# Performance work log

Hardware: AMD Instinct MI355X
Metric: run time of the kernel (lower is better)

The kernel has to match this reference:

```python
import jax, jax.numpy as jnp
import numpy as np

N = 100000      # total nodes in batched graph
E = 1600000     # total edges (avg degree 16)
G = 4096        # number of molecule graphs in the batch
D_IN = 55       # atom feature width (in_features)
H = 128         # hidden_dim
L = 3           # number of GINConv layers


def setup_inputs() -> dict:
    key = jax.random.key(0)
    ks = jax.random.split(key, 10)
    x = jax.random.normal(ks[0], (N, D_IN), dtype=jnp.float32)
    src = jax.random.randint(ks[1], (E,), 0, N)
    dst = jax.random.randint(ks[2], (E,), 0, N)
    graph_ids = jnp.sort(jax.random.randint(ks[3], (N,), 0, G))
    s_in = 1.0 / np.sqrt(D_IN)
    s_h = 1.0 / np.sqrt(H)
    W_fc = jax.random.uniform(ks[4], (D_IN, H), jnp.float32, -s_in, s_in)
    b_fc = jax.random.uniform(ks[5], (H,), jnp.float32, -s_in, s_in)
    W1 = jax.random.uniform(ks[6], (L, H, H), jnp.float32, -s_h, s_h)
    b1 = jax.random.uniform(ks[7], (L, H), jnp.float32, -s_h, s_h)
    W2 = jax.random.uniform(ks[8], (L, H, H), jnp.float32, -s_h, s_h)
    b2 = jax.random.uniform(ks[9], (L, H), jnp.float32, -s_h, s_h)
    return {"x": x, "W_fc": W_fc, "b_fc": b_fc, "W1": W1, "b1": b1,
            "W2": W2, "b2": b2, "src": src, "dst": dst,
            "graph_ids": graph_ids, "n_graphs": G}


def reference(x, W_fc, b_fc, W1, b1, W2, b2, src, dst, graph_ids, n_graphs):
    # node projection: [N, D_IN] -> [N, H]
    h = x @ W_fc + b_fc
    n = h.shape[0]
    for i in range(L):
        agg = jax.ops.segment_sum(h[src], dst, num_segments=n)  # [N, H]
        z = h + agg                                              # (1+eps)*h + agg, eps=0
        z = jnp.maximum(z @ W1[i] + b1[i], 0.0)                  # MLP layer 1 + ReLU
        h = z @ W2[i] + b2[i]                                    # MLP layer 2
    # dgl.sum_nodes: per-graph sum pooling -> [G, H]
    return jax.ops.segment_sum(h, graph_ids, num_segments=n_graphs)
```

## Files before the change

### kernel.cpp

```cpp
#include <hip/hip_runtime.h>

#define DIN 55
#define HD 128
#define EB 8192
#define NBKT 512

typedef unsigned short u16;
typedef unsigned int u32;
typedef _Float16 h8 __attribute__((ext_vector_type(8)));
typedef float f32x4 __attribute__((ext_vector_type(4)));

__device__ __forceinline__ u32 pkh(float a, float b) {
    auto r = __builtin_amdgcn_cvt_pkrtz(a, b);
    union { decltype(r) h; u32 u; } c; c.h = r; return c.u;
}
__device__ __forceinline__ u16 f2h(float v) {
    union { _Float16 f; u16 s; } c; c.f = (_Float16)v; return c.s;
}
__device__ __forceinline__ float h2f(u16 s) {
    union { u16 s; _Float16 f; } c; c.s = s; return (float)c.f;
}
__device__ __forceinline__ float2 h2f2(u32 u) {
    union { u32 v; _Float16 f[2]; } c; c.v = u;
    return make_float2((float)c.f[0], (float)c.f[1]);
}
__device__ __forceinline__ u32 pk8(float a, float b, float c, float d) {
    int p = __builtin_amdgcn_cvt_pk_fp8_f32(a, b, 0, false);
    p = __builtin_amdgcn_cvt_pk_fp8_f32(c, d, p, true);
    return (u32)p;
}
#define ACC8FP8(P, A, B) { \
    auto u0 = __builtin_amdgcn_cvt_pk_f32_fp8((int)(P).x, false); \
    auto u1 = __builtin_amdgcn_cvt_pk_f32_fp8((int)(P).x, true);  \
    auto u2 = __builtin_amdgcn_cvt_pk_f32_fp8((int)(P).y, false); \
    auto u3 = __builtin_amdgcn_cvt_pk_f32_fp8((int)(P).y, true);  \
    A[0] += u0[0]; A[1] += u0[1]; A[2] += u1[0]; A[3] += u1[1];   \
    B[0] += u2[0]; B[1] += u2[1]; B[2] += u3[0]; B[3] += u3[1]; }
__device__ __forceinline__ uint4 up8to16(uint2 p) {
    auto u0 = __builtin_amdgcn_cvt_pk_f32_fp8((int)p.x, false);
    auto u1 = __builtin_amdgcn_cvt_pk_f32_fp8((int)p.x, true);
    auto u2 = __builtin_amdgcn_cvt_pk_f32_fp8((int)p.y, false);
    auto u3 = __builtin_amdgcn_cvt_pk_f32_fp8((int)p.y, true);
    return make_uint4(pkh(u0[0], u0[1]), pkh(u1[0], u1[1]),
                      pkh(u2[0], u2[1]), pkh(u3[0], u3[1]));
}

__global__ __launch_bounds__(256) void prep_kernel(const int* __restrict__ dst,
                                                   int* __restrict__ histT, int E, int nB,
                                                   const float* __restrict__ W1,
                                                   const float* __restrict__ W2,
                                                   const float* __restrict__ Wfc,
                                                   u16* __restrict__ wfrag,
                                                   float* __restrict__ outz, int out_n) {
    __shared__ int hh[NBKT];
    int t = threadIdx.x;
    if (blockIdx.x < (unsigned)nB) {
        int b = blockIdx.x;
        for (int i = t; i < NBKT; i += 256) hh[i] = 0;
        __syncthreads();
        int base = b * EB;
        int end = min(base + EB, E);
        for (int i = base + t; i < end; i += 256) atomicAdd(&hh[dst[i] >> 8], 1);
        __syncthreads();
        for (int k = t; k < NBKT; k += 256) histT[k * nB + b] = hh[k];
        return;
    }
    int bid = blockIdx.x - nB;
    int kc = t >> 6, lane = t & 63;
    if (bid < 48) {
        int m = bid >> 3, ft = bid & 7;
        int l = m >> 1, s = m & 1;
        const float* W = (s ? W2 : W1) + (size_t)l * HD * HD;
        int j = ft * 16 + (lane & 15);
        int k0 = kc * 32 + ((lane >> 4) << 3);
        h8 v;
#pragma unroll
        for (int i = 0; i < 8; i++)
            v[i] = (_Float16)W[(size_t)(k0 + i) * HD + j];
        *(h8*)&wfrag[(((size_t)bid * 4 + kc) * 64 + lane) * 8] = v;
    } else if (bid < 56) {
        if (kc < 2) {
            int ft = bid - 48;
            int j = ft * 16 + (lane & 15);
            int k0 = kc * 32 + ((lane >> 4) << 3);
            h8 v;
#pragma unroll
            for (int i = 0; i < 8; i++) {
                int k = k0 + i;
                v[i] = (k < DIN) ? (_Float16)Wfc[(size_t)k * HD + j] : (_Float16)0.f;
            }
            *(h8*)&wfrag[98304 + (((size_t)(ft * 2 + kc)) * 64 + lane) * 8] = v;
        }
    } else {
        int i = ((bid - 56) * 256 + t) * 2;
        if (i + 1 < out_n) *(float2*)&outz[i] = make_float2(0.f, 0.f);
        else if (i < out_n) outz[i] = 0.f;
    }
}

__global__ __launch_bounds__(256) void scan1_kernel(int* data, int* bsums, int n) {
    __shared__ int sT[256];
    int t = threadIdx.x;
    int base = blockIdx.x * 1024 + t * 4;
    int v0 = (base + 0 < n) ? data[base + 0] : 0;
    int v1 = (base + 1 < n) ? data[base + 1] : 0;
    int v2 = (base + 2 < n) ? data[base + 2] : 0;
    int v3 = (base + 3 < n) ? data[base + 3] : 0;
    v1 += v0; v2 += v1; v3 += v2;
    sT[t] = v3;
    __syncthreads();
    for (int off = 1; off < 256; off <<= 1) {
        int x = (t >= off) ? sT[t - off] : 0;
        __syncthreads();
        sT[t] += x;
        __syncthreads();
    }
    int excl = (t == 0) ? 0 : sT[t - 1];
    if (base + 0 < n) data[base + 0] = v0 + excl;
    if (base + 1 < n) data[base + 1] = v1 + excl;
    if (base + 2 < n) data[base + 2] = v2 + excl;
    if (base + 3 < n) data[base + 3] = v3 + excl;
    if (t == 255) bsums[blockIdx.x] = sT[255];
}

__global__ __launch_bounds__(256) void rpos_kernel(const int* __restrict__ src,
                                                   const int* __restrict__ dst,
                                                   const int* __restrict__ scanned,
                                                   const int* __restrict__ bsums,
                                                   u32* __restrict__ bpairs, int E, int nB,
                                                   int nChunks) {
    __shared__ int sBs[256];
    __shared__ int cur[NBKT];
    int t = threadIdx.x;
    {
        int v = (t < nChunks) ? bsums[t] : 0;
        sBs[t] = v;
        __syncthreads();
        for (int o = 1; o < 256; o <<= 1) {
            int x = (t >= o) ? sBs[t - o] : 0;
            __syncthreads();
            sBs[t] += x;
            __syncthreads();
        }
        sBs[t] -= v;
    }
    __syncthreads();
    for (int b = t; b < NBKT; b += 256) {
        int idx = b * nB + blockIdx.x;
        cur[b] = (idx == 0) ? 0 : scanned[idx - 1] + sBs[(idx - 1) >> 10];
    }
    __syncthreads();
    int base = blockIdx.x * EB;
    int end = min(base + EB, E);
    for (int i = base + t; i < end; i += 256) {
        int d = dst[i];
        int p = atomicAdd(&cur[d >> 8], 1);
        bpairs[p] = ((u32)src[i] << 8) | (u32)(d & 255);
    }
}

__global__ __launch_bounds__(256) void bfinal_kernel(const u32* __restrict__ bpairs,
                                                     const int* __restrict__ scanned,
                                                     const int* __restrict__ bsums,
                                                     int* __restrict__ off,
                                                     int* __restrict__ esrc, int N, int nB,
                                                     int nChunks) {
    __shared__ int sBs[256];
    __shared__ int cnt[256];
    __shared__ int sc[256];
    __shared__ int cur[256];
    int b = blockIdx.x, t = threadIdx.x;
    {
        int v = (t < nChunks) ? bsums[t] : 0;
        sBs[t] = v;
        __syncthreads();
        for (int o = 1; o < 256; o <<= 1) {
            int x = (t >= o) ? sBs[t - o] : 0;
            __syncthreads();
            sBs[t] += x;
            __syncthreads();
        }
        sBs[t] -= v;
    }
    __syncthreads();
    int iLo = b * nB - 1, iHi = (b + 1) * nB - 1;
    int lo = (b == 0) ? 0 : scanned[iLo] + sBs[iLo >> 10];
    int hi = scanned[iHi] + sBs[iHi >> 10];
    cnt[t] = 0;
    __syncthreads();
    for (int i = lo + t; i < hi; i += 256) atomicAdd(&cnt[bpairs[i] & 255u], 1);
    __syncthreads();
    int v = cnt[t];
    sc[t] = v;
    __syncthreads();
    for (int o = 1; o < 256; o <<= 1) {
        int x = (t >= o) ? sc[t - o] : 0;
        __syncthreads();
        sc[t] += x;
        __syncthreads();
    }
    int incl = sc[t];
    int gbase = lo + incl - v;
    int n = b * 256 + t;
    if (n < N) off[n] = gbase;
    if (n == N - 1) off[N] = lo + incl;
    cur[t] = gbase;
    __syncthreads();
    for (int i = lo + t; i < hi; i += 256) {
        u32 p = bpairs[i];
        int q = atomicAdd(&cur[p & 255u], 1);
        esrc[q] = (int)(p >> 8);
    }
}

__global__ __launch_bounds__(256) void agg_kernel(const u32* __restrict__ h8p,
                                                  const int* __restrict__ off,
                                                  const int* __restrict__ esrc,
                                                  u32* __restrict__ z8, int N) {
    int t = threadIdx.x;
    int q = t & 15;
    int n = blockIdx.x * 16 + (t >> 4);
    if (n >= N) return;
    int s0 = off[n], s1 = off[n + 1];
    const int qo = q * 2;
    f32x4 a0 = {0, 0, 0, 0}, b0 = a0, a1 = a0, b1 = a0;
    f32x4 a2 = a0, b2 = a0, a3 = a0, b3 = a0;
    int i = s0;
#define GATH(E, A, B) { uint2 p = *(const uint2*)&h8p[(size_t)(E) * 32 + qo]; ACC8FP8(p, A, B) }
    for (; i + 4 <= s1; i += 4) {
        int e0 = esrc[i + 0], e1 = esrc[i + 1];
        int e2 = esrc[i + 2], e3 = esrc[i + 3];
        GATH(e0, a0, b0) GATH(e1, a1, b1) GATH(e2, a2, b2) GATH(e3, a3, b3)
    }
    if (i + 2 <= s1) {
        int e0 = esrc[i], e1 = esrc[i + 1];
        GATH(e0, a0, b0) GATH(e1, a1, b1)
        i += 2;
    }
    if (i < s1) {
        int e0 = esrc[i];
        GATH(e0, a2, b2)
    }
    GATH(n, a3, b3)
#undef GATH
    f32x4 sa = (a0 + a1) + (a2 + a3);
    f32x4 sb = (b0 + b1) + (b2 + b3);
    *(uint2*)&z8[(size_t)n * 32 + qo] =
        make_uint2(pk8(sa[0], sa[1], sa[2], sa[3]), pk8(sb[0], sb[1], sb[2], sb[3]));
}

__global__ __launch_bounds__(512, 4) void fcm_kernel(const float* __restrict__ x,
                                                     const u16* __restrict__ wfc,
                                                     const float* __restrict__ bfc,
                                                     u32* __restrict__ h8p,
                                                     int N, int nTiles) {
    __shared__ u16 sX[17408];
    const int t = threadIdx.x;
    const int w = t >> 6, lane = t & 63;
    const int col = lane & 15;
    const int fq = lane >> 4;

    h8 aw0 = *(const h8*)&wfc[(((w << 1) + 0) * 64 + lane) * 8];
    h8 aw1 = *(const h8*)&wfc[(((w << 1) + 1) * 64 + lane) * 8];
    float4 bias = *(const float4*)&bfc[w * 16 + fq * 4];

    int tile = blockIdx.x;
    if (tile >= nTiles) return;
    int base = tile * 128;
    int nvalid = min(128, N - base);

    for (int i = t; i < nvalid * DIN; i += 512) {
        float v = x[(size_t)base * DIN + i];
        sX[(i / DIN) * 136 + (i % DIN)] = f2h(v);
    }
    for (int e = t; e < 128 * 9; e += 512)
        sX[(e / 9) * 136 + DIN + (e % 9)] = 0;
    for (int i = nvalid * DIN + t; i < 128 * DIN; i += 512)
        sX[(i / DIN) * 136 + (i % DIN)] = 0;
    __syncthreads();

    f32x4 acc[8];
#pragma unroll
    for (int ntl = 0; ntl < 8; ntl++) {
        int n = ntl * 16 + col;
        h8 b0 = *(const h8*)&sX[n * 136 + fq * 8];
        h8 b1 = *(const h8*)&sX[n * 136 + 32 + fq * 8];
        f32x4 a;
        a[0] = bias.x; a[1] = bias.y; a[2] = bias.z; a[3] = bias.w;
        a = __builtin_amdgcn_mfma_f32_16x16x32_f16(aw0, b0, a, 0, 0, 0);
        a = __builtin_amdgcn_mfma_f32_16x16x32_f16(aw1, b1, a, 0, 0, 0);
        acc[ntl] = a;
    }
    __syncthreads();
#pragma unroll
    for (int ntl = 0; ntl < 8; ntl++) {
        int n = ntl * 16 + col;
        int f = w * 16 + fq * 4;
        *(uint2*)&sX[n * 136 + f] = make_uint2(pkh(acc[ntl][0], acc[ntl][1]),
                                               pkh(acc[ntl][2], acc[ntl][3]));
    }
    __syncthreads();
#pragma unroll
    for (int i = 0; i < 4; i++) {
        int c = t + 512 * i;
        int n = c >> 4, k8 = c & 15;
        if (n < nvalid) {
            uint4 v = *(const uint4*)&sX[n * 136 + k8 * 8];
            float2 f0 = h2f2(v.x), f1 = h2f2(v.y), f2 = h2f2(v.z), f3 = h2f2(v.w);
            *(uint2*)&h8p[(size_t)(base + n) * 32 + k8 * 2] =
                make_uint2(pk8(f0.x, f0.y, f1.x, f1.y), pk8(f2.x, f2.y, f3.x, f3.y));
        }
    }
}

__global__ __launch_bounds__(512, 4) void mlp_pair_kernel(const u32* __restrict__ in8,
                                                          const u16* __restrict__ wf1,
                                                          const u16* __restrict__ wf2,
                                                          const float* __restrict__ b1,
                                                          const float* __restrict__ b2,
                                                          u32* __restrict__ hout,
                                                          const int* __restrict__ gid,
                                                          float* __restrict__ pout,
                                                          int N, int pool) {
    __shared__ u16 sA[8704];
    __shared__ u16 sZ[8704];
    __shared__ int sGid[64];

    const int t = threadIdx.x;
    const int w = t >> 6, lane = t & 63;
    const int col = lane & 15;
    const int fq = lane >> 4;

    const int base = blockIdx.x * 64;
    if (base >= N) return;
    const int nvalid = min(64, N - base);

    h8 aw1[4], aw2[4];
#pragma unroll
    for (int kc = 0; kc < 4; kc++) {
        aw1[kc] = *(const h8*)&wf1[(((w << 2) + kc) << 9) + lane * 8];
        aw2[kc] = *(const h8*)&wf2[(((w << 2) + kc) << 9) + lane * 8];
    }
    float4 bias1 = *(const float4*)&b1[w * 16 + fq * 4];
    float4 bias2 = *(const float4*)&b2[w * 16 + fq * 4];

#pragma unroll
    for (int i = 0; i < 2; i++) {
        int c = t + 512 * i;
        int n = c >> 4, k8 = c & 15;
        uint2 raw = make_uint2(0, 0);
        if (n < nvalid)
            raw = *(const uint2*)&in8[(size_t)(base + n) * 32 + k8 * 2];
        uint4 v16 = up8to16(raw);
        int nt = n >> 4, kc = k8 >> 2;
        int L = ((k8 & 3) << 4) | (n & 15);
        int slot = L ^ (kc << 1);
        *(uint4*)&sA[(((nt << 2) + kc) << 6 | slot) * 8] = v16;
    }
    if (pool && t < 64) sGid[t] = (base + t < N) ? gid[base + t] : 0;
    __syncthreads();

#pragma unroll
    for (int ntl = 0; ntl < 4; ntl++) {
        h8 bx[4];
#pragma unroll
        for (int kc = 0; kc < 4; kc++)
            bx[kc] = *(const h8*)&sA[(((ntl << 2) + kc) << 6 | (lane ^ (kc << 1))) * 8];
        f32x4 a0;
        a0[0] = bias1.x; a0[1] = bias1.y; a0[2] = bias1.z; a0[3] = bias1.w;
#pragma unroll
        for (int kc = 0; kc < 4; kc++)
            a0 = __builtin_amdgcn_mfma_f32_16x16x32_f16(aw1[kc], bx[kc], a0, 0, 0, 0);
        int n = ntl * 16 + col;
        int f = w * 16 + fq * 4;
        u32 lo = pkh(fmaxf(a0[0], 0.f), fmaxf(a0[1], 0.f));
        u32 hi = pkh(fmaxf(a0[2], 0.f), fmaxf(a0[3], 0.f));
        *(uint2*)&sZ[n * 136 + f] = make_uint2(lo, hi);
    }
    __syncthreads();

#pragma unroll
    for (int ntl = 0; ntl < 4; ntl++) {
        int n = ntl * 16 + col;
        h8 bz[4];
#pragma unroll
        for (int kc = 0; kc < 4; kc++)
            bz[kc] = *(const h8*)&sZ[n * 136 + kc * 32 + fq * 8];
        f32x4 a0;
        a0[0] = bias2.x; a0[1] = bias2.y; a0[2] = bias2.z; a0[3] = bias2.w;
#pragma unroll
        for (int kc = 0; kc < 4; kc++)
            a0 = __builtin_amdgcn_mfma_f32_16x16x32_f16(aw2[kc], bz[kc], a0, 0, 0, 0);
        int f = w * 16 + fq * 4;
        *(uint2*)&sA[n * 136 + f] = make_uint2(pkh(a0[0], a0[1]), pkh(a0[2], a0[3]));
    }
    __syncthreads();

    if (!pool) {
#pragma unroll
        for (int i = 0; i < 2; i++) {
            int c = t + 512 * i;
            int n = c >> 4, k8 = c & 15;
            if (n < nvalid) {
                uint4 v = *(const uint4*)&sA[n * 136 + k8 * 8];
                float2 f0 = h2f2(v.x), f1 = h2f2(v.y), f2 = h2f2(v.z), f3 = h2f2(v.w);
                *(uint2*)&hout[(size_t)(base + n) * 32 + k8 * 2] =
                    make_uint2(pk8(f0.x, f0.y, f1.x, f1.y), pk8(f2.x, f2.y, f3.x, f3.y));
            }
        }
    } else {
        int f = t & 127, r = t >> 7;
        int n0 = r * 16;
        if (n0 < nvalid) {
            int nlim = min(n0 + 16, nvalid);
            int curg = sGid[n0];
            float acc = 0.f;
            for (int n = n0; n < nlim; n++) {
                int g = sGid[n];
                if (g != curg) {
                    atomicAdd(&pout[(size_t)curg * HD + f], acc);
                    curg = g; acc = 0.f;
                }
                acc += h2f(sA[n * 136 + f]);
            }
            atomicAdd(&pout[(size_t)curg * HD + f], acc);
        }
    }
}

extern "C" void kernel_launch(void* const* d_in, const int* in_sizes, int n_in,
                              void* d_out, int out_size, void* d_ws, size_t ws_size,
                              hipStream_t stream) {
    (void)n_in; (void)ws_size;
    const float* x   = (const float*)d_in[0];
    const float* Wfc = (const float*)d_in[1];
    const float* bfc = (const float*)d_in[2];
    const float* W1  = (const float*)d_in[3];
    const float* b1  = (const float*)d_in[4];
    const float* W2  = (const float*)d_in[5];
    const float* b2  = (const float*)d_in[6];
    const int* src   = (const int*)d_in[7];
    const int* dst   = (const int*)d_in[8];
    const int* gid   = (const int*)d_in[9];

    int N = in_sizes[0] / DIN;
    int E = in_sizes[7];
    int nTiles = (N + 127) / 128;
    int nTiles64 = (N + 63) / 64;
    int nB = (E + EB - 1) / EB;
    int nScan = NBKT * nB;
    int nChunks = (nScan + 1023) / 1024;

    u32* h8p = (u32*)d_ws;
    u32* z8  = h8p + (size_t)N * 32;
    int* off    = (int*)(z8 + (size_t)N * 32);
    int* esrc   = off + (N + 1);
    int* bsums2 = esrc + E;
    int* histT  = bsums2 + 256;
    u32* bpairs = (u32*)(histT + nScan);
    u16* wfrag  = (u16*)(bpairs + E);

    int zeroBlocks = (out_size + 511) / 512;
    prep_kernel<<<nB + 56 + zeroBlocks, 256, 0, stream>>>(dst, histT, E, nB,
                                                          W1, W2, Wfc, wfrag,
                                                          (float*)d_out, out_size);
    scan1_kernel<<<nChunks, 256, 0, stream>>>(histT, bsums2, nScan);
    rpos_kernel<<<nB, 256, 0, stream>>>(src, dst, histT, bsums2, bpairs, E, nB, nChunks);
    bfinal_kernel<<<NBKT, 256, 0, stream>>>(bpairs, histT, bsums2, off, esrc, N, nB, nChunks);

    fcm_kernel<<<nTiles, 512, 0, stream>>>(x, wfrag + 98304, bfc, h8p, N, nTiles);

    for (int l = 0; l < 3; l++) {
        u16* wf1 = wfrag + (size_t)(2 * l) * 16384;
        u16* wf2 = wf1 + 16384;
        agg_kernel<<<(N + 15) / 16, 256, 0, stream>>>(h8p, off, esrc, z8, N);
        mlp_pair_kernel<<<nTiles64, 512, 0, stream>>>(z8, wf1, wf2,
                                                      b1 + (size_t)l * HD,
                                                      b2 + (size_t)l * HD, h8p,
                                                      gid, (float*)d_out,
                                                      N, (l == 2) ? 1 : 0);
    }
}
```

Baseline: 303.9 us.

## Fuse neighbor aggregation into the GIN MLP kernel with ping-pong buffers

Removes the separate agg_kernel and performs the CSR gather-sum of fp8 neighbor features inside the MLP kernel, writing fp16 results directly into the shared-memory A tile. This skips the fp8 z8 intermediate round trip through global memory and one launch per layer. It also skips the fp8 requantization of the aggregate, which may change precision. Two h buffers alternate because neighbors are read while new h is written. The gather now runs in 512-thread blocks with heavy register use, which may reduce latency hiding.

Result: slower. 337.0 us (+10.9%).

```diff
diff --git a/kernel.cpp b/kernel.cpp
--- a/kernel.cpp
+++ b/kernel.cpp
@@ -36,14 +36,6 @@
     auto u3 = __builtin_amdgcn_cvt_pk_f32_fp8((int)(P).y, true);  \
     A[0] += u0[0]; A[1] += u0[1]; A[2] += u1[0]; A[3] += u1[1];   \
     B[0] += u2[0]; B[1] += u2[1]; B[2] += u3[0]; B[3] += u3[1]; }
-__device__ __forceinline__ uint4 up8to16(uint2 p) {
-    auto u0 = __builtin_amdgcn_cvt_pk_f32_fp8((int)p.x, false);
-    auto u1 = __builtin_amdgcn_cvt_pk_f32_fp8((int)p.x, true);
-    auto u2 = __builtin_amdgcn_cvt_pk_f32_fp8((int)p.y, false);
-    auto u3 = __builtin_amdgcn_cvt_pk_f32_fp8((int)p.y, true);
-    return make_uint4(pkh(u0[0], u0[1]), pkh(u1[0], u1[1]),
-                      pkh(u2[0], u2[1]), pkh(u3[0], u3[1]));
-}
 
 __global__ __launch_bounds__(256) void prep_kernel(const int* __restrict__ dst,
                                                    int* __restrict__ histT, int E, int nB,
@@ -213,42 +205,6 @@
     }
 }
 
-__global__ __launch_bounds__(256) void agg_kernel(const u32* __restrict__ h8p,
-                                                  const int* __restrict__ off,
-                                                  const int* __restrict__ esrc,
-                                                  u32* __restrict__ z8, int N) {
-    int t = threadIdx.x;
-    int q = t & 15;
-    int n = blockIdx.x * 16 + (t >> 4);
-    if (n >= N) return;
-    int s0 = off[n], s1 = off[n + 1];
-    const int qo = q * 2;
-    f32x4 a0 = {0, 0, 0, 0}, b0 = a0, a1 = a0, b1 = a0;
-    f32x4 a2 = a0, b2 = a0, a3 = a0, b3 = a0;
-    int i = s0;
-#define GATH(E, A, B) { uint2 p = *(const uint2*)&h8p[(size_t)(E) * 32 + qo]; ACC8FP8(p, A, B) }
-    for (; i + 4 <= s1; i += 4) {
-        int e0 = esrc[i + 0], e1 = esrc[i + 1];
-        int e2 = esrc[i + 2], e3 = esrc[i + 3];
-        GATH(e0, a0, b0) GATH(e1, a1, b1) GATH(e2, a2, b2) GATH(e3, a3, b3)
-    }
-    if (i + 2 <= s1) {
-        int e0 = esrc[i], e1 = esrc[i + 1];
-        GATH(e0, a0, b0) GATH(e1, a1, b1)
-        i += 2;
-    }
-    if (i < s1) {
-        int e0 = esrc[i];
-        GATH(e0, a2, b2)
-    }
-    GATH(n, a3, b3)
-#undef GATH
-    f32x4 sa = (a0 + a1) + (a2 + a3);
-    f32x4 sb = (b0 + b1) + (b2 + b3);
-    *(uint2*)&z8[(size_t)n * 32 + qo] =
-        make_uint2(pk8(sa[0], sa[1], sa[2], sa[3]), pk8(sb[0], sb[1], sb[2], sb[3]));
-}
-
 __global__ __launch_bounds__(512, 4) void fcm_kernel(const float* __restrict__ x,
                                                      const u16* __restrict__ wfc,
                                                      const float* __restrict__ bfc,
@@ -313,15 +269,17 @@
     }
 }
 
-__global__ __launch_bounds__(512, 4) void mlp_pair_kernel(const u32* __restrict__ in8,
-                                                          const u16* __restrict__ wf1,
-                                                          const u16* __restrict__ wf2,
-                                                          const float* __restrict__ b1,
-                                                          const float* __restrict__ b2,
-                                                          u32* __restrict__ hout,
-                                                          const int* __restrict__ gid,
-                                                          float* __restrict__ pout,
-                                                          int N, int pool) {
+__global__ __launch_bounds__(512, 4) void gin_kernel(const u32* __restrict__ hin,
+                                                     const int* __restrict__ off,
+                                                     const int* __restrict__ esrc,
+                                                     const u16* __restrict__ wf1,
+                                                     const u16* __restrict__ wf2,
+                                                     const float* __restrict__ b1,
+                                                     const float* __restrict__ b2,
+                                                     u32* __restrict__ hout,
+                                                     const int* __restrict__ gid,
+                                                     float* __restrict__ pout,
+                                                     int N, int pool) {
     __shared__ u16 sA[8704];
     __shared__ u16 sZ[8704];
     __shared__ int sGid[64];
@@ -343,21 +301,47 @@
     }
     float4 bias1 = *(const float4*)&b1[w * 16 + fq * 4];
     float4 bias2 = *(const float4*)&b2[w * 16 + fq * 4];
-
-#pragma unroll
-    for (int i = 0; i < 2; i++) {
-        int c = t + 512 * i;
-        int n = c >> 4, k8 = c & 15;
-        uint2 raw = make_uint2(0, 0);
-        if (n < nvalid)
-            raw = *(const uint2*)&in8[(size_t)(base + n) * 32 + k8 * 2];
-        uint4 v16 = up8to16(raw);
-        int nt = n >> 4, kc = k8 >> 2;
-        int L = ((k8 & 3) << 4) | (n & 15);
+    if (pool && t < 64) sGid[t] = (base + t < N) ? gid[base + t] : 0;
+
+    const int q = t & 15;
+    const int qo = q * 2;
+#pragma unroll
+    for (int rep = 0; rep < 2; rep++) {
+        int n_local = (t >> 4) + rep * 32;
+        int n = base + n_local;
+        uint4 v16 = make_uint4(0, 0, 0, 0);
+        if (n < N) {
+            int s0 = off[n], s1 = off[n + 1];
+            f32x4 a0 = {0, 0, 0, 0}, b0 = a0, a1 = a0, b1v = a0;
+            f32x4 a2 = a0, b2v = a0, a3 = a0, b3v = a0;
+            int i = s0;
+#define GATH(E, A, B) { uint2 p = *(const uint2*)&hin[(size_t)(E) * 32 + qo]; ACC8FP8(p, A, B) }
+            for (; i + 4 <= s1; i += 4) {
+                int e0 = esrc[i + 0], e1 = esrc[i + 1];
+                int e2 = esrc[i + 2], e3 = esrc[i + 3];
+                GATH(e0, a0, b0) GATH(e1, a1, b1v) GATH(e2, a2, b2v) GATH(e3, a3, b3v)
+            }
+            if (i + 2 <= s1) {
+                int e0 = esrc[i], e1 = esrc[i + 1];
+                GATH(e0, a0, b0) GATH(e1, a1, b1v)
+                i += 2;
+            }
+            if (i < s1) {
+                int e0 = esrc[i];
+                GATH(e0, a2, b2v)
+            }
+            GATH(n, a3, b3v)
+#undef GATH
+            f32x4 sa = (a0 + a1) + (a2 + a3);
+            f32x4 sb = (b0 + b1v) + (b2v + b3v);
+            v16 = make_uint4(pkh(sa[0], sa[1]), pkh(sa[2], sa[3]),
+                             pkh(sb[0], sb[1]), pkh(sb[2], sb[3]));
+        }
+        int nt = n_local >> 4, kc = q >> 2;
+        int L = ((q & 3) << 4) | (n_local & 15);
         int slot = L ^ (kc << 1);
         *(uint4*)&sA[(((nt << 2) + kc) << 6 | slot) * 8] = v16;
     }
-    if (pool && t < 64) sGid[t] = (base + t < N) ? gid[base + t] : 0;
     __syncthreads();
 
 #pragma unroll
@@ -451,9 +435,9 @@
     int nScan = NBKT * nB;
     int nChunks = (nScan + 1023) / 1024;
 
-    u32* h8p = (u32*)d_ws;
-    u32* z8  = h8p + (size_t)N * 32;
-    int* off    = (int*)(z8 + (size_t)N * 32);
+    u32* h8a = (u32*)d_ws;
+    u32* h8b = h8a + (size_t)N * 32;
+    int* off    = (int*)(h8b + (size_t)N * 32);
     int* esrc   = off + (N + 1);
     int* bsums2 = esrc + E;
     int* histT  = bsums2 + 256;
@@ -468,16 +452,18 @@
     rpos_kernel<<<nB, 256, 0, stream>>>(src, dst, histT, bsums2, bpairs, E, nB, nChunks);
     bfinal_kernel<<<NBKT, 256, 0, stream>>>(bpairs, histT, bsums2, off, esrc, N, nB, nChunks);
 
-    fcm_kernel<<<nTiles, 512, 0, stream>>>(x, wfrag + 98304, bfc, h8p, N, nTiles);
-
+    fcm_kernel<<<nTiles, 512, 0, stream>>>(x, wfrag + 98304, bfc, h8a, N, nTiles);
+
+    u32* hin = h8a;
+    u32* hout = h8b;
     for (int l = 0; l < 3; l++) {
         u16* wf1 = wfrag + (size_t)(2 * l) * 16384;
         u16* wf2 = wf1 + 16384;
-        agg_kernel<<<(N + 15) / 16, 256, 0, stream>>>(h8p, off, esrc, z8, N);
-        mlp_pair_kernel<<<nTiles64, 512, 0, stream>>>(z8, wf1, wf2,
-                                                      b1 + (size_t)l * HD,
-                                                      b2 + (size_t)l * HD, h8p,
-                                                      gid, (float*)d_out,
-                                                      N, (l == 2) ? 1 : 0);
-    }
-}
+        gin_kernel<<<nTiles64, 512, 0, stream>>>(hin, off, esrc, wf1, wf2,
+                                                 b1 + (size_t)l * HD,
+                                                 b2 + (size_t)l * HD, hout,
+                                                 gid, (float*)d_out,
+                                                 N, (l == 2) ? 1 : 0);
+        u32* tmp = hin; hin = hout; hout = tmp;
+    }
+}
```
